# Optimization experiments

Measured on AMD Instinct MI355X. Metric: run time of the kernel, lower is better.

The kernel has to match this reference:

```python
import jax, jax.numpy as jnp
import numpy as np

D_MODEL = 1024
D_STATE = 16
D_CONV = 4
EXPAND = 2
D_INNER = D_MODEL * EXPAND
B_SZ = 2
SEQ = 4096


def setup_inputs() -> dict:
    key = jax.random.key(0)
    ks = jax.random.split(key, 11)
    rn = lambda i, shape, scale=1.0: jax.random.normal(ks[i], shape, jnp.float32) * scale
    return {
        "x": rn(0, (B_SZ, SEQ, D_MODEL)),
        "W_in": rn(1, (D_MODEL, D_INNER), D_MODEL ** -0.5),
        "b_in": rn(2, (D_INNER,), 0.01),
        "conv_w": rn(3, (D_INNER, 1, D_CONV), 0.1),   # torch depthwise layout [out_ch, in_ch/groups=1, k]
        "conv_b": rn(4, (D_INNER,), 0.01),
        # A scaled so tanh(A) is contractive -> stable recurrence over 4096 steps
        "A": rn(5, (D_STATE, D_STATE), 0.1),
        "Bp": rn(6, (D_STATE,)),   # B parameter [d_state, 1] flattened
        "Cp": rn(7, (D_STATE,)),   # C parameter [1, d_state] flattened
        "Dp": rn(8, (1,)),
        "W_out": rn(9, (D_INNER, D_MODEL), D_INNER ** -0.5),
        "b_out": rn(10, (D_MODEL,), 0.01),
    }


def reference(x, W_in, b_in, conv_w, conv_b, A, Bp, Cp, Dp, W_out, b_out):
    Bsz, S, _ = x.shape
    d_inner = W_in.shape[1]
    # input projection
    u = x @ W_in + b_in                              # [B, S, d_inner]
    # causal depthwise conv (torch pads k-1 both sides then slices [:S])
    u = u.transpose(0, 2, 1)                         # [B, d_inner, S]
    u = jax.lax.conv_general_dilated(
        u, conv_w, window_strides=(1,), padding=[(D_CONV - 1, 0)],
        dimension_numbers=("NCH", "OIH", "NCH"),
        feature_group_count=d_inner) + conv_b[None, :, None]
    u = u.transpose(0, 2, 1)                         # [B, S, d_inner]
    # per-channel scalar SSM shared across channels: h_t = tanh(A) h_{t-1} + B u_t; y_t = C h_t + D u_t
    At = jnp.tanh(A)                                 # [ds, ds]
    def step(h, u_t):                                # h: [B, d_inner, ds], u_t: [B, d_inner]
        h = jnp.einsum("ij,bdj->bdi", At, h) + u_t[..., None] * Bp
        y = jnp.einsum("j,bdj->bd", Cp, h) + Dp[0] * u_t
        return h, y
    h0 = jnp.zeros((Bsz, d_inner, Bp.shape[0]), x.dtype)
    _, ys = jax.lax.scan(step, h0, u.transpose(1, 0, 2))  # ys: [S, B, d_inner]
    y = jax.nn.silu(ys.transpose(1, 0, 2))           # [B, S, d_inner]
    return y @ W_out + b_out                         # [B, S, d_model]
```

## Files before the change

kernel.cpp:

```cpp
#include <hip/hip_runtime.h>

typedef unsigned short u16;
typedef float  f32x4  __attribute__((ext_vector_type(4)));
typedef __bf16 bf16x8 __attribute__((ext_vector_type(8)));
typedef u16    u16x4  __attribute__((ext_vector_type(4)));

#define D_MODEL 1024
#define D_INNER 2048
#define B_SZ    2
#define SEQ     4096
#define MROWS   (B_SZ * SEQ)
#define LTAPS   64
#define VROW    136

__device__ __forceinline__ u16 f2bf(float f) {
    return __builtin_bit_cast(u16, (__bf16)f);
}
__device__ __forceinline__ float bf2f(u16 h) {
    unsigned u = ((unsigned)h) << 16;
    return __builtin_bit_cast(float, u);
}

typedef __attribute__((address_space(1))) void gv_t;
typedef __attribute__((address_space(3))) void lv_t;
__device__ __forceinline__ void glds16(const u16* g, u16* l) {
    __builtin_amdgcn_global_load_lds((gv_t*)g, (lv_t*)l, 16, 0, 0);
}
__device__ __forceinline__ void wait_vm0() { __builtin_amdgcn_s_waitcnt(0x0F70); }

__device__ __forceinline__ void transpose_tile(
    const float* __restrict__ in, u16* __restrict__ out,
    int R, int C, int c0, int r0, int tid, float (*tile)[33])
{
    const int tx = tid & 31, ty = tid >> 5;
    for (int k = 0; k < 32; k += 8)
        tile[ty + k][tx] = in[(size_t)(r0 + ty + k) * C + c0 + tx];
    __syncthreads();
    for (int k = 0; k < 32; k += 8)
        out[(size_t)(c0 + ty + k) * R + r0 + tx] = f2bf(tile[tx][ty + k]);
}

__global__ __launch_bounds__(256) void prep_kernel(
    const float* __restrict__ x, u16* __restrict__ xb,
    const float* __restrict__ Win, u16* __restrict__ WinT,
    const float* __restrict__ Wout, u16* __restrict__ WoutT,
    const float* __restrict__ A, const float* __restrict__ Bp,
    const float* __restrict__ Cp, const float* __restrict__ Dp,
    u16* __restrict__ Amat64)
{
    __shared__ float tile[32][33];
    __shared__ float fs[LTAPS];
    const int bx = blockIdx.x, tid = threadIdx.x;
    if (bx < 8192) {
        size_t i = ((size_t)bx * 256 + tid) * 4;
        f32x4 v = *(const f32x4*)(x + i);
        u16x4 o;
        o.x = f2bf(v.x); o.y = f2bf(v.y); o.z = f2bf(v.z); o.w = f2bf(v.w);
        *(u16x4*)(xb + i) = o;
    } else if (bx < 10240) {
        const int flat = bx - 8192;
        transpose_tile(Win, WinT, 1024, 2048,
                       (flat & 63) * 32, (flat >> 6) * 32, tid, tile);
    } else if (bx < 12288) {
        const int flat = bx - 10240;
        transpose_tile(Wout, WoutT, 2048, 1024,
                       (flat & 31) * 32, (flat >> 5) * 32, tid, tile);
    } else {
        if (tid < 64) {
            const int i = tid & 15;
            float Atr[16];
            for (int j = 0; j < 16; j++) Atr[j] = tanhf(A[i * 16 + j]);
            float p = Bp[i];
            const float c  = Cp[i];
            const float d0 = Dp[0];
            for (int t = 0; t < LTAPS; t++) {
                float fv = c * p;
                fv += __shfl_xor(fv, 1); fv += __shfl_xor(fv, 2);
                fv += __shfl_xor(fv, 4); fv += __shfl_xor(fv, 8);
                if (tid == 0) fs[t] = fv + (t == 0 ? d0 : 0.f);
                float n0 = 0.f, n1 = 0.f, n2 = 0.f, n3 = 0.f;
                #pragma unroll
                for (int j = 0; j < 4; j++) {
                    n0 = fmaf(Atr[j],      __shfl(p, j),      n0);
                    n1 = fmaf(Atr[j + 4],  __shfl(p, j + 4),  n1);
                    n2 = fmaf(Atr[j + 8],  __shfl(p, j + 8),  n2);
                    n3 = fmaf(Atr[j + 12], __shfl(p, j + 12), n3);
                }
                p = (n0 + n1) + (n2 + n3);
            }
        }
        __syncthreads();
        for (int idx = tid; idx < 64 * 128; idx += 256) {
            const int i = idx >> 7, j = idx & 127;
            const int tau = 64 + i - j;
            float v = (tau >= 0 && tau < LTAPS) ? fs[tau] : 0.f;
            Amat64[idx] = f2bf(v);
        }
    }
}

template <int MODE>
__global__ __launch_bounds__(256) void gemm_bt_kernel(
    const u16* __restrict__ A, const u16* __restrict__ BT,
    void* __restrict__ Cout, const float* __restrict__ bias,
    int M, int N, int K)
{
    __shared__ u16 As[128 * 32];
    __shared__ u16 Bs[128 * 32];
    const int tid = threadIdx.x, lane = tid & 63, wid = tid >> 6;
    const int nTiles = gridDim.x;
    const int bid = blockIdx.x + nTiles * blockIdx.y;
    const int xcd = bid & 7;
    const int loc = bid >> 3;
    const int mt  = xcd * (gridDim.y >> 3) + (loc & 7);
    const int nt  = loc >> 3;
    const int m0 = mt * 128, n0 = nt * 128;
    const int sr = wid * 32 + (lane >> 2);
    const int sc = (lane & 3) * 8;
    const u16* ga = A  + (size_t)(m0 + sr) * K + sc;
    const u16* gb = BT + (size_t)(n0 + sr) * K + sc;
    u16* la = As + wid * 1024;
    u16* lb = Bs + wid * 1024;
    const int wm = (wid & 1) * 64, wn = (wid >> 1) * 64;
    const int fr = lane & 15, fq = lane >> 4;
    f32x4 acc[4][4] = {};
    for (int k0 = 0; k0 < K; k0 += 32) {
        glds16(ga + k0, la);
        glds16(ga + k0 + (size_t)16 * K, la + 512);
        glds16(gb + k0, lb);
        glds16(gb + k0 + (size_t)16 * K, lb + 512);
        wait_vm0();
        __syncthreads();
        bf16x8 af[4], bfr[4];
        for (int i = 0; i < 4; i++)
            af[i]  = *(const bf16x8*)(As + (wm + i * 16 + fr) * 32 + fq * 8);
        for (int i = 0; i < 4; i++)
            bfr[i] = *(const bf16x8*)(Bs + (wn + i * 16 + fr) * 32 + fq * 8);
        for (int mi = 0; mi < 4; mi++)
            for (int ni = 0; ni < 4; ni++)
                acc[mi][ni] = __builtin_amdgcn_mfma_f32_16x16x32_bf16(
                    bfr[ni], af[mi], acc[mi][ni], 0, 0, 0);
        __syncthreads();
    }
    for (int ni = 0; ni < 4; ni++) {
        const int colb = n0 + wn + ni * 16 + fq * 4;
        const f32x4 bv = *(const f32x4*)(bias + colb);
        for (int mi = 0; mi < 4; mi++) {
            const int row = m0 + wm + mi * 16 + fr;
            f32x4 v = acc[mi][ni];
            v.x += bv.x; v.y += bv.y; v.z += bv.z; v.w += bv.w;
            if constexpr (MODE == 0) {
                u16x4 o;
                o.x = f2bf(v.x); o.y = f2bf(v.y); o.z = f2bf(v.z); o.w = f2bf(v.w);
                *(u16x4*)((u16*)Cout + (size_t)row * N + colb) = o;
            } else {
                *(f32x4*)((float*)Cout + (size_t)row * N + colb) = v;
            }
        }
    }
}

__global__ __launch_bounds__(256) void conv_fir_mfma_kernel(
    const u16* __restrict__ u, const float* __restrict__ cw,
    const float* __restrict__ cb, const u16* __restrict__ Amat64,
    u16* __restrict__ Y)
{
    __shared__ u16 VT[128 * VROW];
    const int tid = threadIdx.x;
    const int c0 = blockIdx.x * 128, t0 = blockIdx.y * 64, b = blockIdx.z;
    {
        const int tx = tid & 127, ty = tid >> 7;
        const int cg = c0 + tx;
        const float w0 = cw[cg * 4 + 0], w1 = cw[cg * 4 + 1];
        const float w2 = cw[cg * 4 + 2], w3 = cw[cg * 4 + 3];
        const float cbv = cb[cg];
        const u16* ucol = u + (size_t)b * SEQ * D_INNER + cg;
        const int s0 = t0 - 64 + ty * 64;
        u16* vrow = VT + tx * VROW + ty * 64;
        if (s0 + 63 < 0) {
            const u16x4 z = {0, 0, 0, 0};
            #pragma unroll
            for (int j = 0; j < 16; j++) *(u16x4*)(vrow + j * 4) = z;
        } else {
            float xm3 = (s0 - 3 >= 0) ? bf2f(ucol[(size_t)(s0 - 3) * D_INNER]) : 0.f;
            float xm2 = (s0 - 2 >= 0) ? bf2f(ucol[(size_t)(s0 - 2) * D_INNER]) : 0.f;
            float xm1 = (s0 - 1 >= 0) ? bf2f(ucol[(size_t)(s0 - 1) * D_INNER]) : 0.f;
            #pragma unroll 4
            for (int j = 0; j < 16; j++) {
                const u16* p = ucol + (size_t)(s0 + j * 4) * D_INNER;
                float x0 = bf2f(p[0]);
                float x1 = bf2f(p[(size_t)D_INNER]);
                float x2 = bf2f(p[(size_t)2 * D_INNER]);
                float x3 = bf2f(p[(size_t)3 * D_INNER]);
                u16x4 o;
                o.x = f2bf(cbv + w0 * xm3 + w1 * xm2 + w2 * xm1 + w3 * x0);
                o.y = f2bf(cbv + w0 * xm2 + w1 * xm1 + w2 * x0  + w3 * x1);
                o.z = f2bf(cbv + w0 * xm1 + w1 * x0  + w2 * x1  + w3 * x2);
                o.w = f2bf(cbv + w0 * x0  + w1 * x1  + w2 * x2  + w3 * x3);
                *(u16x4*)(vrow + j * 4) = o;
                xm3 = x1; xm2 = x2; xm1 = x3;
            }
        }
    }
    __syncthreads();
    const int lane = tid & 63, wid = tid >> 6;
    const int wm = (wid & 1) * 32, wn = (wid >> 1) * 64;
    const int fr = lane & 15, fq = lane >> 4;
    f32x4 acc[2][4] = {};
    #pragma unroll
    for (int kq = 0; kq < 4; kq++) {
        const int k0 = kq * 32;
        bf16x8 af[2], bfr[4];
        #pragma unroll
        for (int mi = 0; mi < 2; mi++)
            af[mi] = *(const bf16x8*)(Amat64 + (wm + mi * 16 + fr) * 128 + k0 + fq * 8);
        #pragma unroll
        for (int ni = 0; ni < 4; ni++)
            bfr[ni] = *(const bf16x8*)(VT + (wn + ni * 16 + fr) * VROW + k0 + fq * 8);
        #pragma unroll
        for (int mi = 0; mi < 2; mi++)
            #pragma unroll
            for (int ni = 0; ni < 4; ni++)
                acc[mi][ni] = __builtin_amdgcn_mfma_f32_16x16x32_bf16(
                    bfr[ni], af[mi], acc[mi][ni], 0, 0, 0);
    }
    #pragma unroll
    for (int ni = 0; ni < 4; ni++) {
        const int cbase = c0 + wn + ni * 16 + fq * 4;
        #pragma unroll
        for (int mi = 0; mi < 2; mi++) {
            const int trow = t0 + wm + mi * 16 + fr;
            f32x4 v = acc[mi][ni];
            u16x4 o;
            o.x = f2bf(v.x / (1.f + __expf(-v.x)));
            o.y = f2bf(v.y / (1.f + __expf(-v.y)));
            o.z = f2bf(v.z / (1.f + __expf(-v.z)));
            o.w = f2bf(v.w / (1.f + __expf(-v.w)));
            *(u16x4*)(Y + ((size_t)(b * SEQ + trow)) * D_INNER + cbase) = o;
        }
    }
}

extern "C" void kernel_launch(void* const* d_in, const int* in_sizes, int n_in,
                              void* d_out, int out_size, void* d_ws, size_t ws_size,
                              hipStream_t stream)
{
    const float* x    = (const float*)d_in[0];
    const float* Win  = (const float*)d_in[1];
    const float* bin  = (const float*)d_in[2];
    const float* cw   = (const float*)d_in[3];
    const float* cb   = (const float*)d_in[4];
    const float* A    = (const float*)d_in[5];
    const float* Bp   = (const float*)d_in[6];
    const float* Cp   = (const float*)d_in[7];
    const float* Dp   = (const float*)d_in[8];
    const float* Wout = (const float*)d_in[9];
    const float* bout = (const float*)d_in[10];
    float* out = (float*)d_out;

    char* ws = (char*)d_ws;
    u16* xb     = (u16*)(ws);
    u16* WinT   = (u16*)(ws + 16777216);
    u16* WoutT  = (u16*)(ws + 20971520);
    u16* u      = (u16*)(ws + 25165824);
    u16* Y      = (u16*)(ws + 58720256);
    u16* Amat64 = (u16*)(ws + 92274688);

    prep_kernel<<<12289, 256, 0, stream>>>(x, xb, Win, WinT, Wout, WoutT,
                                           A, Bp, Cp, Dp, Amat64);
    gemm_bt_kernel<0><<<dim3(16, 64), 256, 0, stream>>>(xb, WinT, u, bin,
                                                        MROWS, D_INNER, D_MODEL);
    conv_fir_mfma_kernel<<<dim3(16, 64, 2), 256, 0, stream>>>(u, cw, cb, Amat64, Y);
    gemm_bt_kernel<1><<<dim3(8, 64), 256, 0, stream>>>(Y, WoutT, out, bout,
                                                       MROWS, D_MODEL, D_INNER);
}
```

Before: 265.0 us.

## Prefetch next GEMM K-tile during MFMA and vectorize conv loads over channel pairs

The GEMM loop now issues the global-to-LDS loads for the next K slice right after the current fragments are read into registers. Those loads then overlap the MFMA work, replacing the load-wait-compute-sync pattern with split waitcnt and barrier steps. The conv/FIR prologue is also restructured: each thread handles two adjacent channels with 32-bit loads and a shorter time span, which halves the number of scalar global loads. The risks are that the hand-placed waitcnt and barrier ordering must be right to avoid LDS races, and that the zero-fill condition was rewritten.

```diff
diff --git a/kernel.cpp b/kernel.cpp
--- a/kernel.cpp
+++ b/kernel.cpp
@@ -3,6 +3,7 @@
 typedef unsigned short u16;
 typedef float  f32x4  __attribute__((ext_vector_type(4)));
 typedef __bf16 bf16x8 __attribute__((ext_vector_type(8)));
+typedef u16    u16x2  __attribute__((ext_vector_type(2)));
 typedef u16    u16x4  __attribute__((ext_vector_type(4)));
 
 #define D_MODEL 1024
@@ -26,7 +27,8 @@
 __device__ __forceinline__ void glds16(const u16* g, u16* l) {
     __builtin_amdgcn_global_load_lds((gv_t*)g, (lv_t*)l, 16, 0, 0);
 }
-__device__ __forceinline__ void wait_vm0() { __builtin_amdgcn_s_waitcnt(0x0F70); }
+#define WAIT_VM0   0x0F70
+#define WAIT_LGKM0 0xC07F
 
 __device__ __forceinline__ void transpose_tile(
     const float* __restrict__ in, u16* __restrict__ out,
@@ -124,23 +126,37 @@
     const int wm = (wid & 1) * 64, wn = (wid >> 1) * 64;
     const int fr = lane & 15, fq = lane >> 4;
     f32x4 acc[4][4] = {};
-    for (int k0 = 0; k0 < K; k0 += 32) {
-        glds16(ga + k0, la);
-        glds16(ga + k0 + (size_t)16 * K, la + 512);
-        glds16(gb + k0, lb);
-        glds16(gb + k0 + (size_t)16 * K, lb + 512);
-        wait_vm0();
-        __syncthreads();
+    glds16(ga, la);
+    glds16(ga + (size_t)16 * K, la + 512);
+    glds16(gb, lb);
+    glds16(gb + (size_t)16 * K, lb + 512);
+    const int iters = K >> 5;
+    for (int it = 0; it < iters; ++it) {
+        __builtin_amdgcn_s_waitcnt(WAIT_VM0);
+        __builtin_amdgcn_s_barrier();
         bf16x8 af[4], bfr[4];
+        #pragma unroll
         for (int i = 0; i < 4; i++)
             af[i]  = *(const bf16x8*)(As + (wm + i * 16 + fr) * 32 + fq * 8);
+        #pragma unroll
         for (int i = 0; i < 4; i++)
             bfr[i] = *(const bf16x8*)(Bs + (wn + i * 16 + fr) * 32 + fq * 8);
+        asm volatile("" ::: "memory");
+        __builtin_amdgcn_s_waitcnt(WAIT_LGKM0);
+        __builtin_amdgcn_s_barrier();
+        if (it + 1 < iters) {
+            const int k0 = (it + 1) << 5;
+            glds16(ga + k0, la);
+            glds16(ga + k0 + (size_t)16 * K, la + 512);
+            glds16(gb + k0, lb);
+            glds16(gb + k0 + (size_t)16 * K, lb + 512);
+        }
+        #pragma unroll
         for (int mi = 0; mi < 4; mi++)
+            #pragma unroll
             for (int ni = 0; ni < 4; ni++)
                 acc[mi][ni] = __builtin_amdgcn_mfma_f32_16x16x32_bf16(
                     bfr[ni], af[mi], acc[mi][ni], 0, 0, 0);
-        __syncthreads();
     }
     for (int ni = 0; ni < 4; ni++) {
         const int colb = n0 + wn + ni * 16 + fq * 4;
@@ -169,36 +185,57 @@
     const int tid = threadIdx.x;
     const int c0 = blockIdx.x * 128, t0 = blockIdx.y * 64, b = blockIdx.z;
     {
-        const int tx = tid & 127, ty = tid >> 7;
-        const int cg = c0 + tx;
-        const float w0 = cw[cg * 4 + 0], w1 = cw[cg * 4 + 1];
-        const float w2 = cw[cg * 4 + 2], w3 = cw[cg * 4 + 3];
-        const float cbv = cb[cg];
+        const int tx = tid & 63, ty = tid >> 6;
+        const int cg = c0 + tx * 2;
+        const f32x4 wA = *(const f32x4*)(cw + cg * 4);
+        const f32x4 wB = *(const f32x4*)(cw + cg * 4 + 4);
+        const float cb0 = cb[cg], cb1 = cb[cg + 1];
         const u16* ucol = u + (size_t)b * SEQ * D_INNER + cg;
-        const int s0 = t0 - 64 + ty * 64;
-        u16* vrow = VT + tx * VROW + ty * 64;
-        if (s0 + 63 < 0) {
+        const int s0 = t0 - 64 + ty * 32;
+        u16* vr0 = VT + (tx * 2)     * VROW + ty * 32;
+        u16* vr1 = VT + (tx * 2 + 1) * VROW + ty * 32;
+        if (t0 == 0 && ty < 2) {
             const u16x4 z = {0, 0, 0, 0};
             #pragma unroll
-            for (int j = 0; j < 16; j++) *(u16x4*)(vrow + j * 4) = z;
+            for (int j = 0; j < 8; j++) {
+                *(u16x4*)(vr0 + j * 4) = z;
+                *(u16x4*)(vr1 + j * 4) = z;
+            }
         } else {
-            float xm3 = (s0 - 3 >= 0) ? bf2f(ucol[(size_t)(s0 - 3) * D_INNER]) : 0.f;
-            float xm2 = (s0 - 2 >= 0) ? bf2f(ucol[(size_t)(s0 - 2) * D_INNER]) : 0.f;
-            float xm1 = (s0 - 1 >= 0) ? bf2f(ucol[(size_t)(s0 - 1) * D_INNER]) : 0.f;
-            #pragma unroll 4
-            for (int j = 0; j < 16; j++) {
+            float am3 = 0.f, am2 = 0.f, am1 = 0.f;
+            float bm3 = 0.f, bm2 = 0.f, bm1 = 0.f;
+            if (s0 > 0) {
+                u16x2 d3 = *(const u16x2*)(ucol + (size_t)(s0 - 3) * D_INNER);
+                u16x2 d2 = *(const u16x2*)(ucol + (size_t)(s0 - 2) * D_INNER);
+                u16x2 d1 = *(const u16x2*)(ucol + (size_t)(s0 - 1) * D_INNER);
+                am3 = bf2f(d3.x); bm3 = bf2f(d3.y);
+                am2 = bf2f(d2.x); bm2 = bf2f(d2.y);
+                am1 = bf2f(d1.x); bm1 = bf2f(d1.y);
+            }
+            #pragma unroll 2
+            for (int j = 0; j < 8; j++) {
                 const u16* p = ucol + (size_t)(s0 + j * 4) * D_INNER;
-                float x0 = bf2f(p[0]);
-                float x1 = bf2f(p[(size_t)D_INNER]);
-                float x2 = bf2f(p[(size_t)2 * D_INNER]);
-                float x3 = bf2f(p[(size_t)3 * D_INNER]);
-                u16x4 o;
-                o.x = f2bf(cbv + w0 * xm3 + w1 * xm2 + w2 * xm1 + w3 * x0);
-                o.y = f2bf(cbv + w0 * xm2 + w1 * xm1 + w2 * x0  + w3 * x1);
-                o.z = f2bf(cbv + w0 * xm1 + w1 * x0  + w2 * x1  + w3 * x2);
-                o.w = f2bf(cbv + w0 * x0  + w1 * x1  + w2 * x2  + w3 * x3);
-                *(u16x4*)(vrow + j * 4) = o;
-                xm3 = x1; xm2 = x2; xm1 = x3;
+                u16x2 r0 = *(const u16x2*)(p);
+                u16x2 r1 = *(const u16x2*)(p + (size_t)D_INNER);
+                u16x2 r2 = *(const u16x2*)(p + (size_t)2 * D_INNER);
+                u16x2 r3 = *(const u16x2*)(p + (size_t)3 * D_INNER);
+                float a0 = bf2f(r0.x), b0 = bf2f(r0.y);
+                float a1 = bf2f(r1.x), b1 = bf2f(r1.y);
+                float a2 = bf2f(r2.x), b2 = bf2f(r2.y);
+                float a3 = bf2f(r3.x), b3 = bf2f(r3.y);
+                u16x4 oa, ob;
+                oa.x = f2bf(cb0 + wA.x * am3 + wA.y * am2 + wA.z * am1 + wA.w * a0);
+                oa.y = f2bf(cb0 + wA.x * am2 + wA.y * am1 + wA.z * a0  + wA.w * a1);
+                oa.z = f2bf(cb0 + wA.x * am1 + wA.y * a0  + wA.z * a1  + wA.w * a2);
+                oa.w = f2bf(cb0 + wA.x * a0  + wA.y * a1  + wA.z * a2  + wA.w * a3);
+                ob.x = f2bf(cb1 + wB.x * bm3 + wB.y * bm2 + wB.z * bm1 + wB.w * b0);
+                ob.y = f2bf(cb1 + wB.x * bm2 + wB.y * bm1 + wB.z * b0  + wB.w * b1);
+                ob.z = f2bf(cb1 + wB.x * bm1 + wB.y * b0  + wB.z * b1  + wB.w * b2);
+                ob.w = f2bf(cb1 + wB.x * b0  + wB.y * b1  + wB.z * b2  + wB.w * b3);
+                *(u16x4*)(vr0 + j * 4) = oa;
+                *(u16x4*)(vr1 + j * 4) = ob;
+                am3 = a1; am2 = a2; am1 = a3;
+                bm3 = b1; bm2 = b2; bm1 = b3;
             }
         }
     }
```

Result: faster. 241.1 us (-9.0%).
